# Kernel tuning notes

Hardware: AMD Instinct MI355X
Metric: run time of the kernel (lower is better)

## Reference

```python
import jax, jax.numpy as jnp
import numpy as np

B, T, N, IN, H, K = 8, 10, 50, 6, 256, 4
E = N * (N - 1)


def setup_inputs() -> dict:
    key = jax.random.key(0)
    ks = jax.random.split(key, 22)
    p = lambda k, shape: jax.random.normal(k, shape, jnp.float32) * 0.05
    return {
        "inputs": jax.random.normal(ks[0], (B, T, N, IN), jnp.float32),
        "sampled_edges": jax.random.uniform(ks[1], (B, T, E, K), dtype=jnp.float32),
        "msg_w1": p(ks[2], (K, H, 2 * H)), "msg_b1": p(ks[3], (K, H)),
        "msg_w2": p(ks[4], (K, H, H)), "msg_b2": p(ks[5], (K, H)),
        "w_hr": p(ks[6], (H, H)), "w_hi": p(ks[7], (H, H)), "w_hh": p(ks[8], (H, H)),
        "w_ir": p(ks[9], (H, IN)), "b_ir": p(ks[10], (H,)),
        "w_ii": p(ks[11], (H, IN)), "b_ii": p(ks[12], (H,)),
        "w_in": p(ks[13], (H, IN)), "b_in": p(ks[14], (H,)),
        "w_o1": p(ks[15], (H, H)), "b_o1": p(ks[16], (H,)),
        "w_o2": p(ks[17], (H, H)), "b_o2": p(ks[18], (H,)),
        "w_o3": p(ks[19], (IN, H)), "b_o3": p(ks[20], (IN,)),
    }


def reference(inputs, sampled_edges, msg_w1, msg_b1, msg_w2, msg_b2,
              w_hr, w_hi, w_hh, w_ir, b_ir, w_ii, b_ii, w_in, b_in,
              w_o1, b_o1, w_o2, b_o2, w_o3, b_o3):
    b, t, n, _ = inputs.shape
    k = msg_w1.shape[0]
    h = msg_w1.shape[1]
    # fully-connected directed graph, no self loops (static indices)
    send_np, recv_np = np.where(np.ones((n, n)) - np.eye(n))
    send = jnp.asarray(send_np)
    recv = jnp.asarray(recv_np)
    norm = float(k) - 1.0  # skip_first_edge_type = True

    def single_step(ins, rel, hidden):
        # ins: [B,N,IN], rel: [B,E,K], hidden: [B,N,H]
        pre = jnp.concatenate([hidden[:, recv], hidden[:, send]], axis=-1)  # [B,E,2H]
        all_msgs = jnp.zeros((b, pre.shape[1], h), inputs.dtype)
        for i in range(1, k):  # skip first edge type
            m = jnp.tanh(jnp.einsum('bef,hf->beh', pre, msg_w1[i]) + msg_b1[i])
            m = jnp.tanh(jnp.einsum('beh,jh->bej', m, msg_w2[i]) + msg_b2[i])
            all_msgs = all_msgs + m * rel[:, :, i:i + 1] / norm
        # scatter-add messages to receiver nodes (replaces onehot matmul)
        agg = jnp.zeros((b, n, h), inputs.dtype).at[:, recv].add(all_msgs) / (n - 1)
        r = jax.nn.sigmoid(ins @ w_ir.T + b_ir + agg @ w_hr.T)
        ig = jax.nn.sigmoid(ins @ w_ii.T + b_ii + agg @ w_hi.T)
        nn_ = jnp.tanh(ins @ w_in.T + b_in + r * (agg @ w_hh.T))
        hidden = (1 - ig) * nn_ + ig * hidden
        pred = jax.nn.relu(hidden @ w_o1.T + b_o1)
        pred = jax.nn.relu(pred @ w_o2.T + b_o2)
        pred = ins + (pred @ w_o3.T + b_o3)
        return pred, hidden

    x_t = jnp.swapaxes(inputs, 0, 1)         # [T,B,N,IN]
    e_t = jnp.swapaxes(sampled_edges, 0, 1)  # [T,B,E,K]
    h0 = jnp.zeros((b, n, h), inputs.dtype)

    def step(carry, xs):
        hidden, prev = carry
        xt, et, s = xs
        ins = jnp.where(s == 0, xt, prev)  # teacher_forcing=False: only step 0 uses inputs
        pred, hidden = single_step(ins, et, hidden)
        return (hidden, pred), pred

    _, preds = jax.lax.scan(step, (h0, jnp.zeros_like(x_t[0])), (x_t, e_t, jnp.arange(t)))
    return jnp.swapaxes(preds, 0, 1)  # [B,T,N,IN]
```

## Files before the change

### kernel.cpp

```cpp
#include <hip/hip_runtime.h>
#include <hip/hip_bf16.h>
#include <stdint.h>

#define B_ 8
#define T_ 10
#define N_ 50
#define IN_ 6
#define H_ 256
#define K_ 4
#define E_ 2450
#define ROWS 400
#define AP 102400

typedef __attribute__((ext_vector_type(8))) __bf16 bf16x8;
typedef __attribute__((ext_vector_type(4))) float f32x4;

__device__ __forceinline__ unsigned short f2bf(float x) {
    unsigned int u = __float_as_uint(x);
    u = (u + 0x7fffu + ((u >> 16) & 1u)) >> 16;
    return (unsigned short)u;
}
__device__ __forceinline__ unsigned pk2(float a, float b) {
    return (unsigned)f2bf(a) | ((unsigned)f2bf(b) << 16);
}
__device__ __forceinline__ float rcp_fast(float x) { return __builtin_amdgcn_rcpf(x); }
__device__ __forceinline__ float tanh_fast(float x) {
    float e = __expf(2.0f * x);
    return 1.0f - 2.0f * rcp_fast(e + 1.0f);
}
__device__ __forceinline__ float sigmoid_fast(float x) {
    return rcp_fast(1.0f + __expf(-x));
}

__global__ __launch_bounds__(256) void swizzle_weights(
        const float* __restrict__ w1, const float* __restrict__ w2,
        const float* __restrict__ whr, const float* __restrict__ whi,
        const float* __restrict__ whh, const float* __restrict__ wo1,
        const float* __restrict__ wo2, const float* __restrict__ b1,
        unsigned short* __restrict__ w1s, unsigned short* __restrict__ w2s,
        unsigned short* __restrict__ gws, unsigned short* __restrict__ wos,
        unsigned int* __restrict__ hidden_zero, float* __restrict__ UV) {
    const int W1N = 3 * 16 * 16 * 64 * 8;
    const int W2N = 3 * 16 * 8 * 64 * 8;
    const int GWN = 3 * 65536;
    const int WON = 2 * 65536;
    const int ZN  = 102400;
    int idx = blockIdx.x * 256 + threadIdx.x;
    if (idx < W1N) {
        int j = idx & 7, L = (idx >> 3) & 63, kt = (idx >> 9) & 15;
        int nt = (idx >> 13) & 15, i = idx >> 17;
        int n = nt * 16 + (L & 15);
        int k = kt * 32 + ((L >> 4) << 3) + j;
        w1s[idx] = f2bf(w1[((size_t)(i + 1) * H_ + n) * (2 * H_) + k]);
    } else if (idx < W1N + W2N) {
        int t = idx - W1N;
        int j = t & 7, L = (t >> 3) & 63, kt = (t >> 9) & 7;
        int nt = (t >> 12) & 15, i = t >> 16;
        int n = nt * 16 + (L & 15);
        int k = kt * 32 + ((L >> 4) << 3) + j;
        w2s[t] = f2bf(w2[((size_t)(i + 1) * H_ + n) * H_ + k]);
    } else if (idx < W1N + W2N + GWN) {
        int t = idx - (W1N + W2N);
        int j = t & 7, L = (t >> 3) & 63, kt = (t >> 9) & 7;
        int nt = (t >> 12) & 15, mat = t >> 16;
        int n = nt * 16 + (L & 15);
        int k = kt * 32 + ((L >> 4) << 3) + j;
        const float* src = (mat == 0) ? whr : (mat == 1) ? whi : whh;
        gws[t] = f2bf(src[(size_t)n * H_ + k]);
    } else if (idx < W1N + W2N + GWN + WON) {
        int t = idx - (W1N + W2N + GWN);
        int j = t & 7, L = (t >> 3) & 63, kt = (t >> 9) & 7;
        int nt = (t >> 12) & 15, g = t >> 16;
        int n = nt * 16 + (L & 15);
        int k = kt * 32 + ((L >> 4) << 3) + j;
        const float* src = (g == 0) ? wo1 : wo2;
        wos[t] = f2bf(src[(size_t)n * H_ + k]);
    } else if (idx < W1N + W2N + GWN + WON + ZN) {
        hidden_zero[idx - (W1N + W2N + GWN + WON)] = 0u;
    } else {
        int t = idx - (W1N + W2N + GWN + WON + ZN);
        int c = t & 511;
        int ty = (t >> 9) % 3;
        UV[t] = (c < 256) ? b1[(ty + 1) * H_ + c] : 0.0f;
    }
}

__global__ __launch_bounds__(256, 4) void msgagg_kernel(
        const float* __restrict__ UV, const float* __restrict__ edges,
        const unsigned short* __restrict__ w2s,
        const float* __restrict__ b2, float* __restrict__ aggP, int t) {
    __shared__ unsigned short m1F[32 * 512];
    __shared__ float relS[64];

    int ty = blockIdx.x / 400;
    int rem = blockIdx.x - ty * 400;
    int b = rem / 50;
    int r = rem - b * 50;
    int tid = threadIdx.x;
    int lane = tid & 63, wid = tid >> 6;
    int col = lane & 15, q = lane >> 4;

    if (tid < 64) {
        float v = 0.0f;
        if (tid < 50 && tid != r) {
            int e = tid * 49 + (r > tid ? r - 1 : r);
            v = edges[(((size_t)b * T_ + t) * E_ + e) * K_ + ty + 1];
        }
        relS[tid] = v;
    }

    {
        int row = wid * 16 + col;
        int sv = row < N_ ? row : N_ - 1;
        const float* Vrow = &UV[((size_t)(b * N_ + sv) * 3 + ty) * 512 + 256 + q * 8];
        const float* Urow = &UV[((size_t)(b * N_ + r) * 3 + ty) * 512 + q * 8];
        #pragma unroll
        for (int kt = 0; kt < 8; ++kt) {
            float4 v0 = *(const float4*)(Vrow + kt * 32);
            float4 v1 = *(const float4*)(Vrow + kt * 32 + 4);
            float4 u0 = *(const float4*)(Urow + kt * 32);
            float4 u1 = *(const float4*)(Urow + kt * 32 + 4);
            float m0 = tanh_fast(u0.x + v0.x);
            float m1 = tanh_fast(u0.y + v0.y);
            float m2 = tanh_fast(u0.z + v0.z);
            float m3 = tanh_fast(u0.w + v0.w);
            float m4 = tanh_fast(u1.x + v1.x);
            float m5 = tanh_fast(u1.y + v1.y);
            float m6 = tanh_fast(u1.z + v1.z);
            float m7 = tanh_fast(u1.w + v1.w);
            uint4 pk;
            pk.x = pk2(m0, m1); pk.y = pk2(m2, m3);
            pk.z = pk2(m4, m5); pk.w = pk2(m6, m7);
            *(uint4*)&m1F[(wid * 8 + kt) * 512 + lane * 8] = pk;
        }
    }
    __syncthreads();

    const bf16x8* w2f = (const bf16x8*)w2s;
    f32x4 acc[4][4];
    #pragma unroll
    for (int mt = 0; mt < 4; ++mt)
        #pragma unroll
        for (int u = 0; u < 4; ++u) acc[mt][u] = (f32x4){0.f, 0.f, 0.f, 0.f};

    #pragma unroll
    for (int kt = 0; kt < 8; ++kt) {
        bf16x8 a0 = *(const bf16x8*)&m1F[(0 * 8 + kt) * 512 + lane * 8];
        bf16x8 a1 = *(const bf16x8*)&m1F[(1 * 8 + kt) * 512 + lane * 8];
        bf16x8 a2 = *(const bf16x8*)&m1F[(2 * 8 + kt) * 512 + lane * 8];
        bf16x8 a3 = *(const bf16x8*)&m1F[(3 * 8 + kt) * 512 + lane * 8];
        #pragma unroll
        for (int u = 0; u < 4; ++u) {
            bf16x8 w = w2f[(size_t)((ty * 16 + wid * 4 + u) * 8 + kt) * 64 + lane];
            acc[0][u] = __builtin_amdgcn_mfma_f32_16x16x32_bf16(a0, w, acc[0][u], 0, 0, 0);
            acc[1][u] = __builtin_amdgcn_mfma_f32_16x16x32_bf16(a1, w, acc[1][u], 0, 0, 0);
            acc[2][u] = __builtin_amdgcn_mfma_f32_16x16x32_bf16(a2, w, acc[2][u], 0, 0, 0);
            acc[3][u] = __builtin_amdgcn_mfma_f32_16x16x32_bf16(a3, w, acc[3][u], 0, 0, 0);
        }
    }
    #pragma unroll
    for (int u = 0; u < 4; ++u) {
        float bias = b2[(ty + 1) * H_ + (wid * 4 + u) * 16 + col];
        float sum = 0.0f;
        #pragma unroll
        for (int mt = 0; mt < 4; ++mt)
            #pragma unroll
            for (int rg = 0; rg < 4; ++rg) {
                int row = mt * 16 + q * 4 + rg;
                sum += tanh_fast(acc[mt][u][rg] + bias) * relS[row];
            }
        sum += __shfl_xor(sum, 16);
        sum += __shfl_xor(sum, 32);
        if (lane < 16)
            aggP[(size_t)ty * AP + (size_t)(b * N_ + r) * H_ +
                 (wid * 4 + u) * 16 + col] = sum * (1.0f / 147.0f);
    }
}

__global__ __launch_bounds__(512, 2) void nodeuv_kernel(
        const float* __restrict__ inputs, const float* __restrict__ aggP,
        const unsigned short* __restrict__ gws, const unsigned short* __restrict__ wos,
        const unsigned short* __restrict__ w1s,
        const float* __restrict__ hid_rd, float* __restrict__ hid_wr,
        float* __restrict__ UV,
        const float* __restrict__ w_ir, const float* __restrict__ b_ir,
        const float* __restrict__ w_ii, const float* __restrict__ b_ii,
        const float* __restrict__ w_in, const float* __restrict__ b_in,
        const float* __restrict__ b1,
        const float* __restrict__ b_o1, const float* __restrict__ b_o2,
        const float* __restrict__ w_o3, const float* __restrict__ b_o3,
        float* __restrict__ out, int t) {
    __shared__ unsigned short aggF[8 * 512];
    __shared__ unsigned short hnF[8 * 512];
    __shared__ unsigned short p1F[8 * 512];
    __shared__ float p2L[16 * 260];
    __shared__ float insS[16 * 6];

    int role = blockIdx.x / 25;
    int mm = blockIdx.x - role * 25;
    if (role > 0 && t == T_ - 1) return;

    int tid = threadIdx.x;
    int lane = tid & 63, wid = tid >> 6;
    int col = lane & 15, q = lane >> 4;

    const float* src = (t == 0) ? inputs : out;
    int tt = (t == 0) ? 0 : (t - 1);

    {
        int kt = tid >> 6, L = tid & 63;
        int row = mm * 16 + (L & 15);
        int k0 = kt * 32 + ((L >> 4) << 3);
        const float* p = &aggP[(size_t)row * H_ + k0];
        float4 a0 = *(const float4*)(p);
        float4 a1 = *(const float4*)(p + 4);
        float4 b0 = *(const float4*)(p + AP);
        float4 b1v = *(const float4*)(p + AP + 4);
        float4 c0 = *(const float4*)(p + 2 * AP);
        float4 c1 = *(const float4*)(p + 2 * AP + 4);
        uint4 pk;
        pk.x = pk2(a0.x + b0.x + c0.x, a0.y + b0.y + c0.y);
        pk.y = pk2(a0.z + b0.z + c0.z, a0.w + b0.w + c0.w);
        pk.z = pk2(a1.x + b1v.x + c1.x, a1.y + b1v.y + c1.y);
        pk.w = pk2(a1.z + b1v.z + c1.z, a1.w + b1v.w + c1.w);
        *(uint4*)&aggF[(size_t)kt * 512 + L * 8] = pk;
    }
    if (tid < 96) {
        int rl = tid / 6, c = tid - rl * 6;
        int row = mm * 16 + rl;
        int b = row / 50, n = row - b * 50;
        insS[rl * 6 + c] = src[(((size_t)b * T_ + tt) * N_ + n) * IN_ + c];
    }
    __syncthreads();

    const bf16x8* gwf = (const bf16x8*)gws;
    bf16x8 af[8];
    #pragma unroll
    for (int kt = 0; kt < 8; ++kt)
        af[kt] = *(const bf16x8*)&aggF[kt * 512 + lane * 8];

    f32x4 acc[3][2];
    #pragma unroll
    for (int m = 0; m < 3; ++m)
        #pragma unroll
        for (int u = 0; u < 2; ++u) acc[m][u] = (f32x4){0.f, 0.f, 0.f, 0.f};

    bf16x8 wg[2][2][3][2];
    #pragma unroll
    for (int ki = 0; ki < 2; ++ki)
        #pragma unroll
        for (int m = 0; m < 3; ++m)
            #pragma unroll
            for (int u = 0; u < 2; ++u)
                wg[0][ki][m][u] = gwf[(size_t)((m * 16 + wid * 2 + u) * 8 + ki) * 64 + lane];
    #pragma unroll
    for (int c = 0; c < 4; ++c) {
        if (c < 3) {
            #pragma unroll
            for (int ki = 0; ki < 2; ++ki)
                #pragma unroll
                for (int m = 0; m < 3; ++m)
                    #pragma unroll
                    for (int u = 0; u < 2; ++u)
                        wg[(c + 1) & 1][ki][m][u] =
                            gwf[(size_t)((m * 16 + wid * 2 + u) * 8 + (c + 1) * 2 + ki) * 64 + lane];
        }
        #pragma unroll
        for (int ki = 0; ki < 2; ++ki)
            #pragma unroll
            for (int m = 0; m < 3; ++m)
                #pragma unroll
                for (int u = 0; u < 2; ++u)
                    acc[m][u] = __builtin_amdgcn_mfma_f32_16x16x32_bf16(
                        af[c * 2 + ki], wg[c & 1][ki][m][u], acc[m][u], 0, 0, 0);
    }

    const bf16x8* wof = (const bf16x8*)wos;
    const bf16x8* w1f = (const bf16x8*)w1s;
    bf16x8 tw[8][2];
    if (role == 0) {
        #pragma unroll
        for (int kt = 0; kt < 8; ++kt)
            #pragma unroll
            for (int u = 0; u < 2; ++u)
                tw[kt][u] = wof[(size_t)((wid * 2 + u) * 8 + kt) * 64 + lane];
    } else {
        int ty = role - 1;
        #pragma unroll
        for (int kt = 0; kt < 8; ++kt)
            #pragma unroll
            for (int u = 0; u < 2; ++u)
                tw[kt][u] = w1f[(size_t)((ty * 16 + wid * 2 + u) * 16 + kt) * 64 + lane];
    }

    #pragma unroll
    for (int u = 0; u < 2; ++u) {
        int h = (wid * 2 + u) * 16 + col;
        float bir = b_ir[h], bii = b_ii[h], bin_ = b_in[h];
        float wir[6], wii[6], win[6];
        #pragma unroll
        for (int c = 0; c < 6; ++c) {
            wir[c] = w_ir[h * 6 + c];
            wii[c] = w_ii[h * 6 + c];
            win[c] = w_in[h * 6 + c];
        }
        #pragma unroll
        for (int rg = 0; rg < 4; ++rg) {
            int rl = q * 4 + rg;
            int row = mm * 16 + rl;
            float xr = bir, xi = bii, xn = bin_;
            #pragma unroll
            for (int c = 0; c < 6; ++c) {
                float iv = insS[rl * 6 + c];
                xr += wir[c] * iv;
                xi += wii[c] * iv;
                xn += win[c] * iv;
            }
            float rgate = sigmoid_fast(xr + acc[0][u][rg]);
            float igate = sigmoid_fast(xi + acc[1][u][rg]);
            float nn = tanh_fast(xn + rgate * acc[2][u][rg]);
            size_t off = (size_t)row * H_ + h;
            float hold = hid_rd[off];
            float hnew = (1.0f - igate) * nn + igate * hold;
            if (role == 0) hid_wr[off] = hnew;
            hnF[(h >> 5) * 512 + (((h >> 3) & 3) * 16 + rl) * 8 + (h & 7)] = f2bf(hnew);
        }
    }
    __syncthreads();

    if (role > 0) {
        int ty = role - 1;
        bf16x8 a2f[8];
        #pragma unroll
        for (int kt = 0; kt < 8; ++kt)
            a2f[kt] = *(const bf16x8*)&hnF[kt * 512 + lane * 8];
        bf16x8 wv1[8][2];
        #pragma unroll
        for (int kt = 0; kt < 8; ++kt)
            #pragma unroll
            for (int u = 0; u < 2; ++u)
                wv1[kt][u] = w1f[(size_t)((ty * 16 + wid * 2 + u) * 16 + 8 + kt) * 64 + lane];
        f32x4 acc0[2], acc1[2];
        #pragma unroll
        for (int u = 0; u < 2; ++u) {
            acc0[u] = (f32x4){0.f, 0.f, 0.f, 0.f};
            acc1[u] = (f32x4){0.f, 0.f, 0.f, 0.f};
        }
        #pragma unroll
        for (int kt = 0; kt < 8; ++kt)
            #pragma unroll
            for (int u = 0; u < 2; ++u)
                acc0[u] = __builtin_amdgcn_mfma_f32_16x16x32_bf16(a2f[kt], tw[kt][u], acc0[u], 0, 0, 0);
        #pragma unroll
        for (int kt = 0; kt < 8; ++kt)
            #pragma unroll
            for (int u = 0; u < 2; ++u)
                acc1[u] = __builtin_amdgcn_mfma_f32_16x16x32_bf16(a2f[kt], wv1[kt][u], acc1[u], 0, 0, 0);
        #pragma unroll
        for (int u = 0; u < 2; ++u) {
            int nt = wid * 2 + u;
            float bias = b1[(ty + 1) * H_ + nt * 16 + col];
            #pragma unroll
            for (int r = 0; r < 4; ++r) {
                size_t base = ((size_t)(mm * 16 + q * 4 + r) * 3 + ty) * 512 + nt * 16 + col;
                UV[base] = acc0[u][r] + bias;
                UV[base + 256] = acc1[u][r];
            }
        }
        return;
    }

    {
        bf16x8 a1f[8];
        #pragma unroll
        for (int kt = 0; kt < 8; ++kt)
            a1f[kt] = *(const bf16x8*)&hnF[kt * 512 + lane * 8];
        bf16x8 o2w[8][2];
        #pragma unroll
        for (int kt = 0; kt < 8; ++kt)
            #pragma unroll
            for (int u = 0; u < 2; ++u)
                o2w[kt][u] = wof[(size_t)((16 + wid * 2 + u) * 8 + kt) * 64 + lane];
        f32x4 a1v[2];
        #pragma unroll
        for (int u = 0; u < 2; ++u) a1v[u] = (f32x4){0.f, 0.f, 0.f, 0.f};
        #pragma unroll
        for (int kt = 0; kt < 8; ++kt)
            #pragma unroll
            for (int u = 0; u < 2; ++u)
                a1v[u] = __builtin_amdgcn_mfma_f32_16x16x32_bf16(a1f[kt], tw[kt][u], a1v[u], 0, 0, 0);
        #pragma unroll
        for (int u = 0; u < 2; ++u) {
            int h = (wid * 2 + u) * 16 + col;
            float bo = b_o1[h];
            #pragma unroll
            for (int rg = 0; rg < 4; ++rg) {
                int rl = q * 4 + rg;
                float v = fmaxf(a1v[u][rg] + bo, 0.0f);
                p1F[(h >> 5) * 512 + (((h >> 3) & 3) * 16 + rl) * 8 + (h & 7)] = f2bf(v);
            }
        }
        __syncthreads();

        bf16x8 a2f[8];
        #pragma unroll
        for (int kt = 0; kt < 8; ++kt)
            a2f[kt] = *(const bf16x8*)&p1F[kt * 512 + lane * 8];
        f32x4 a2v[2];
        #pragma unroll
        for (int u = 0; u < 2; ++u) a2v[u] = (f32x4){0.f, 0.f, 0.f, 0.f};
        #pragma unroll
        for (int kt = 0; kt < 8; ++kt)
            #pragma unroll
            for (int u = 0; u < 2; ++u)
                a2v[u] = __builtin_amdgcn_mfma_f32_16x16x32_bf16(a2f[kt], o2w[kt][u], a2v[u], 0, 0, 0);
        #pragma unroll
        for (int u = 0; u < 2; ++u) {
            int h = (wid * 2 + u) * 16 + col;
            float bo = b_o2[h];
            #pragma unroll
            for (int rg = 0; rg < 4; ++rg) {
                int rl = q * 4 + rg;
                p2L[rl * 260 + h] = fmaxf(a2v[u][rg] + bo, 0.0f);
            }
        }
    }
    __syncthreads();

    if (tid < 192) {
        int o = tid >> 3;
        int part = tid & 7;
        #pragma unroll
        for (int pass = 0; pass < 4; ++pass) {
            int oo = o + pass * 24;
            int rl = oo / 6, c = oo - rl * 6;
            float acc3 = (part == 0) ? b_o3[c] : 0.0f;
            const float* wrow = &w_o3[c * 256];
            const float* prow = &p2L[rl * 260];
            #pragma unroll
            for (int i = 0; i < 8; ++i) {
                int k = i * 32 + part * 4;
                float4 w = *(const float4*)&wrow[k];
                float4 p = *(const float4*)&prow[k];
                acc3 += w.x * p.x + w.y * p.y + w.z * p.z + w.w * p.w;
            }
            acc3 += __shfl_xor(acc3, 1);
            acc3 += __shfl_xor(acc3, 2);
            acc3 += __shfl_xor(acc3, 4);
            if (part == 0) {
                int row = mm * 16 + rl;
                int b = row / 50, n = row - b * 50;
                out[(((size_t)b * T_ + t) * N_ + n) * IN_ + c] = insS[rl * 6 + c] + acc3;
            }
        }
    }
}

extern "C" void kernel_launch(void* const* d_in, const int* in_sizes, int n_in,
                              void* d_out, int out_size, void* d_ws, size_t ws_size,
                              hipStream_t stream) {
    const float* inputs = (const float*)d_in[0];
    const float* edges  = (const float*)d_in[1];
    const float* msg_w1 = (const float*)d_in[2];
    const float* msg_b1 = (const float*)d_in[3];
    const float* msg_w2 = (const float*)d_in[4];
    const float* msg_b2 = (const float*)d_in[5];
    const float* w_hr = (const float*)d_in[6];
    const float* w_hi = (const float*)d_in[7];
    const float* w_hh = (const float*)d_in[8];
    const float* w_ir = (const float*)d_in[9];
    const float* b_ir = (const float*)d_in[10];
    const float* w_ii = (const float*)d_in[11];
    const float* b_ii = (const float*)d_in[12];
    const float* w_in = (const float*)d_in[13];
    const float* b_in = (const float*)d_in[14];
    const float* w_o1 = (const float*)d_in[15];
    const float* b_o1 = (const float*)d_in[16];
    const float* w_o2 = (const float*)d_in[17];
    const float* b_o2 = (const float*)d_in[18];
    const float* w_o3 = (const float*)d_in[19];
    const float* b_o3 = (const float*)d_in[20];
    float* out = (float*)d_out;

    char* ws = (char*)d_ws;
    float* hidden0           = (float*)(ws);
    float* hidden1           = (float*)(ws + 409600);
    float* UV                = (float*)(ws + 819200);
    float* aggP              = (float*)(ws + 3276800);
    unsigned short* w1s      = (unsigned short*)(ws + 4505600);
    unsigned short* w2s      = (unsigned short*)(ws + 5292032);
    unsigned short* gws      = (unsigned short*)(ws + 5685248);
    unsigned short* wos      = (unsigned short*)(ws + 6078464);

    swizzle_weights<<<dim3(6384), dim3(256), 0, stream>>>(
        msg_w1, msg_w2, w_hr, w_hi, w_hh, w_o1, w_o2, msg_b1,
        w1s, w2s, gws, wos, (unsigned int*)hidden0, UV);

    float* hid[2] = {hidden0, hidden1};
    for (int t = 0; t < T_; ++t) {
        msgagg_kernel<<<dim3(1200), dim3(256), 0, stream>>>(
            UV, edges, w2s, msg_b2, aggP, t);
        nodeuv_kernel<<<dim3(100), dim3(512), 0, stream>>>(
            inputs, aggP, gws, wos, w1s, hid[t & 1], hid[(t + 1) & 1], UV,
            w_ir, b_ir, w_ii, b_ii, w_in, b_in, msg_b1,
            b_o1, b_o2, w_o3, b_o3, out, t);
    }
}
```

Baseline: 499.0 us.

## Split nodeuv U/V projections across more blocks and prefetch hidden and weights early

The nodeuv grid grows from 100 to 175 blocks, so each role>0 block computes only one half (U or V) of one edge type's first-layer projection instead of both. The GRU projection gate work, which every block recomputes, is therefore duplicated across more blocks. The previous hidden state and the tail-stage weights are now loaded before the gate MFMA loop so their latency overlaps the math. The occupancy hint of 2 blocks per CU is removed from launch bounds, giving the compiler more register room at some cost in occupancy.

```diff
diff --git a/kernel.cpp b/kernel.cpp
--- a/kernel.cpp
+++ b/kernel.cpp
@@ -177,7 +177,7 @@
     }
 }
 
-__global__ __launch_bounds__(512, 2) void nodeuv_kernel(
+__global__ __launch_bounds__(512) void nodeuv_kernel(
         const float* __restrict__ inputs, const float* __restrict__ aggP,
         const unsigned short* __restrict__ gws, const unsigned short* __restrict__ wos,
         const unsigned short* __restrict__ w1s,
@@ -239,6 +239,36 @@
     for (int kt = 0; kt < 8; ++kt)
         af[kt] = *(const bf16x8*)&aggF[kt * 512 + lane * 8];
 
+    float hpre[2][4];
+    #pragma unroll
+    for (int u = 0; u < 2; ++u) {
+        int h = (wid * 2 + u) * 16 + col;
+        #pragma unroll
+        for (int rg = 0; rg < 4; ++rg) {
+            int row = mm * 16 + q * 4 + rg;
+            hpre[u][rg] = hid_rd[(size_t)row * H_ + h];
+        }
+    }
+
+    const bf16x8* wof = (const bf16x8*)wos;
+    const bf16x8* w1f = (const bf16x8*)w1s;
+    bf16x8 tw[8][2];
+    if (role == 0) {
+        #pragma unroll
+        for (int kt = 0; kt < 8; ++kt)
+            #pragma unroll
+            for (int u = 0; u < 2; ++u)
+                tw[kt][u] = wof[(size_t)((wid * 2 + u) * 8 + kt) * 64 + lane];
+    } else {
+        int s = role - 1;
+        int ty = s >> 1, half = s & 1;
+        #pragma unroll
+        for (int kt = 0; kt < 8; ++kt)
+            #pragma unroll
+            for (int u = 0; u < 2; ++u)
+                tw[kt][u] = w1f[(size_t)((ty * 16 + wid * 2 + u) * 16 + half * 8 + kt) * 64 + lane];
+    }
+
     f32x4 acc[3][2];
     #pragma unroll
     for (int m = 0; m < 3; ++m)
@@ -273,24 +303,6 @@
                 for (int u = 0; u < 2; ++u)
                     acc[m][u] = __builtin_amdgcn_mfma_f32_16x16x32_bf16(
                         af[c * 2 + ki], wg[c & 1][ki][m][u], acc[m][u], 0, 0, 0);
-    }
-
-    const bf16x8* wof = (const bf16x8*)wos;
-    const bf16x8* w1f = (const bf16x8*)w1s;
-    bf16x8 tw[8][2];
-    if (role == 0) {
-        #pragma unroll
-        for (int kt = 0; kt < 8; ++kt)
-            #pragma unroll
-            for (int u = 0; u < 2; ++u)
-                tw[kt][u] = wof[(size_t)((wid * 2 + u) * 8 + kt) * 64 + lane];
-    } else {
-        int ty = role - 1;
-        #pragma unroll
-        for (int kt = 0; kt < 8; ++kt)
-            #pragma unroll
-            for (int u = 0; u < 2; ++u)
-                tw[kt][u] = w1f[(size_t)((ty * 16 + wid * 2 + u) * 16 + kt) * 64 + lane];
     }
 
     #pragma unroll
@@ -319,53 +331,36 @@
             float rgate = sigmoid_fast(xr + acc[0][u][rg]);
             float igate = sigmoid_fast(xi + acc[1][u][rg]);
             float nn = tanh_fast(xn + rgate * acc[2][u][rg]);
-            size_t off = (size_t)row * H_ + h;
-            float hold = hid_rd[off];
-            float hnew = (1.0f - igate) * nn + igate * hold;
-            if (role == 0) hid_wr[off] = hnew;
+            float hnew = (1.0f - igate) * nn + igate * hpre[u][rg];
+            if (role == 0) hid_wr[(size_t)row * H_ + h] = hnew;
             hnF[(h >> 5) * 512 + (((h >> 3) & 3) * 16 + rl) * 8 + (h & 7)] = f2bf(hnew);
         }
     }
     __syncthreads();
 
     if (role > 0) {
-        int ty = role - 1;
+        int s = role - 1;
+        int ty = s >> 1, half = s & 1;
         bf16x8 a2f[8];
         #pragma unroll
         for (int kt = 0; kt < 8; ++kt)
             a2f[kt] = *(const bf16x8*)&hnF[kt * 512 + lane * 8];
-        bf16x8 wv1[8][2];
-        #pragma unroll
-        for (int kt = 0; kt < 8; ++kt)
-            #pragma unroll
-            for (int u = 0; u < 2; ++u)
-                wv1[kt][u] = w1f[(size_t)((ty * 16 + wid * 2 + u) * 16 + 8 + kt) * 64 + lane];
-        f32x4 acc0[2], acc1[2];
-        #pragma unroll
-        for (int u = 0; u < 2; ++u) {
-            acc0[u] = (f32x4){0.f, 0.f, 0.f, 0.f};
-            acc1[u] = (f32x4){0.f, 0.f, 0.f, 0.f};
-        }
-        #pragma unroll
-        for (int kt = 0; kt < 8; ++kt)
-            #pragma unroll
-            for (int u = 0; u < 2; ++u)
-                acc0[u] = __builtin_amdgcn_mfma_f32_16x16x32_bf16(a2f[kt], tw[kt][u], acc0[u], 0, 0, 0);
-        #pragma unroll
-        for (int kt = 0; kt < 8; ++kt)
-            #pragma unroll
-            for (int u = 0; u < 2; ++u)
-                acc1[u] = __builtin_amdgcn_mfma_f32_16x16x32_bf16(a2f[kt], wv1[kt][u], acc1[u], 0, 0, 0);
+        f32x4 acc2[2];
+        #pragma unroll
+        for (int u = 0; u < 2; ++u) acc2[u] = (f32x4){0.f, 0.f, 0.f, 0.f};
+        #pragma unroll
+        for (int kt = 0; kt < 8; ++kt)
+            #pragma unroll
+            for (int u = 0; u < 2; ++u)
+                acc2[u] = __builtin_amdgcn_mfma_f32_16x16x32_bf16(a2f[kt], tw[kt][u], acc2[u], 0, 0, 0);
         #pragma unroll
         for (int u = 0; u < 2; ++u) {
             int nt = wid * 2 + u;
-            float bias = b1[(ty + 1) * H_ + nt * 16 + col];
-            #pragma unroll
-            for (int r = 0; r < 4; ++r) {
-                size_t base = ((size_t)(mm * 16 + q * 4 + r) * 3 + ty) * 512 + nt * 16 + col;
-                UV[base] = acc0[u][r] + bias;
-                UV[base + 256] = acc1[u][r];
-            }
+            float bias = (half == 0) ? b1[(ty + 1) * H_ + nt * 16 + col] : 0.0f;
+            #pragma unroll
+            for (int r = 0; r < 4; ++r)
+                UV[((size_t)(mm * 16 + q * 4 + r) * 3 + ty) * 512 + half * 256 +
+                   nt * 16 + col] = acc2[u][r] + bias;
         }
         return;
     }
@@ -500,7 +495,7 @@
     for (int t = 0; t < T_; ++t) {
         msgagg_kernel<<<dim3(1200), dim3(256), 0, stream>>>(
             UV, edges, w2s, msg_b2, aggP, t);
-        nodeuv_kernel<<<dim3(100), dim3(512), 0, stream>>>(
+        nodeuv_kernel<<<dim3(175), dim3(512), 0, stream>>>(
             inputs, aggP, gws, wos, w1s, hid[t & 1], hid[(t + 1) & 1], UV,
             w_ir, b_ir, w_ii, b_ii, w_in, b_in, msg_b1,
             b_o1, b_o2, w_o3, b_o3, out, t);
```

Result: faster. 487.3 us (median of 2 runs) (-2.4%).
